# Kernel tuning notes

Hardware: AMD Instinct MI355X
Metric: run time of the kernel (lower is better)

Reference implementation:

```python
import jax, jax.numpy as jnp
import numpy as np

B = 8192
CNN_DIM = 2048
MLP_DIM = 2048
HID = 1024
H = 16
D = HID // H  # 64
EPS = 1e-5


def setup_inputs() -> dict:
    key = jax.random.key(0)
    ks = jax.random.split(key, 12)
    s = 0.02
    return {
        'cnn_out': jax.random.normal(ks[0], (B, CNN_DIM), jnp.float32),
        'mlp_out': jax.random.normal(ks[1], (B, MLP_DIM), jnp.float32),
        # weights stored [in, out] (transposed vs torch nn.Linear)
        'W_cqkv': jax.random.normal(ks[2], (CNN_DIM, 3 * HID), jnp.float32) * s,
        'b_cqkv': jnp.zeros((3 * HID,), jnp.float32),
        'W_mqkv': jax.random.normal(ks[3], (MLP_DIM, 3 * HID), jnp.float32) * s,
        'b_mqkv': jnp.zeros((3 * HID,), jnp.float32),
        'g1': jnp.ones((HID,), jnp.float32),
        'be1': jnp.zeros((HID,), jnp.float32),
        'g2': jnp.ones((HID,), jnp.float32),
        'be2': jnp.zeros((HID,), jnp.float32),
        'W_cproj': jax.random.normal(ks[4], (HID, CNN_DIM), jnp.float32) * s,
        'b_cproj': jnp.zeros((CNN_DIM,), jnp.float32),
        'W_mproj': jax.random.normal(ks[5], (HID, MLP_DIM), jnp.float32) * s,
        'b_mproj': jnp.zeros((MLP_DIM,), jnp.float32),
    }


def _layernorm(x, g, b):
    m = jnp.mean(x, axis=-1, keepdims=True)
    v = jnp.mean((x - m) ** 2, axis=-1, keepdims=True)
    return (x - m) / jnp.sqrt(v + EPS) * g + b


def reference(cnn_out, mlp_out, W_cqkv, b_cqkv, W_mqkv, b_mqkv,
              g1, be1, g2, be2, W_cproj, b_cproj, W_mproj, b_mproj):
    bsz = cnn_out.shape[0]
    scale = 1.0 / jnp.sqrt(jnp.float32(D))

    cqkv = (cnn_out @ W_cqkv + b_cqkv).reshape(bsz, 3, H, D)
    cq, ck, cv = cqkv[:, 0], cqkv[:, 1], cqkv[:, 2]  # each [B,H,D]
    mqkv = (mlp_out @ W_mqkv + b_mqkv).reshape(bsz, 3, H, D)
    mq, mk, mv = mqkv[:, 0], mqkv[:, 1], mqkv[:, 2]

    # branch 1: cnn queries attend over mlp heads -> [B,H,H]
    a1 = jax.nn.softmax(jnp.einsum('bhd,bgd->bhg', cq, mk) * scale, axis=-1)
    ca = jnp.einsum('bhg,bgd->bhd', a1, mv)
    # torch: transpose(1,2).view(B, hidden) -> [B, D, H] flattened
    ca = jnp.swapaxes(ca, 1, 2).reshape(bsz, HID)
    cnn_enh = cnn_out + _layernorm(ca, g1, be1) @ W_cproj + b_cproj

    # branch 2: mlp queries attend over cnn heads
    a2 = jax.nn.softmax(jnp.einsum('bhd,bgd->bhg', mq, ck) * scale, axis=-1)
    ma = jnp.einsum('bhg,bgd->bhd', a2, cv)
    ma = jnp.swapaxes(ma, 1, 2).reshape(bsz, HID)
    mlp_enh = mlp_out + _layernorm(ma, g2, be2) @ W_mproj + b_mproj

    return (cnn_enh, mlp_enh)
```

## Files before the change

kernel.cpp:

```cpp
#include <hip/hip_runtime.h>
#include <hip/hip_bf16.h>
#include <cstdint>
#include <cstddef>

#define NROWS 8192
#define DIM   2048
#define HIDN  1024
#define QKV3  3072
#define EPSV  1e-5f

typedef __attribute__((ext_vector_type(8))) short bf16x8;
typedef __attribute__((ext_vector_type(4))) float f32x4;

__device__ __forceinline__ unsigned short f2bf(float x) {
    __hip_bfloat16 h = __float2bfloat16(x);
    return *reinterpret_cast<unsigned short*>(&h);
}
__device__ __forceinline__ float bf2f(unsigned short u) {
    return __uint_as_float((unsigned)u << 16);
}

__device__ __forceinline__ void gload_lds16(const void* g, void* l) {
    __builtin_amdgcn_global_load_lds(
        (const __attribute__((address_space(1))) void*)g,
        (__attribute__((address_space(3))) void*)l, 16, 0, 0);
}

template <int N> __device__ __forceinline__ void vmwait() {
    if constexpr (N == 8)      asm volatile("s_waitcnt vmcnt(8)" ::: "memory");
    else if constexpr (N == 4) asm volatile("s_waitcnt vmcnt(4)" ::: "memory");
    else if constexpr (N == 2) asm volatile("s_waitcnt vmcnt(2)" ::: "memory");
    else if constexpr (N == 0) asm volatile("s_waitcnt vmcnt(0)" ::: "memory");
}
__device__ __forceinline__ void barrier_mem() {
    asm volatile("s_barrier" ::: "memory");
}

__global__ __launch_bounds__(256) void cvt2_f32_bf16(const float* __restrict__ inA,
                                                     unsigned short* __restrict__ outA,
                                                     const float* __restrict__ inB,
                                                     unsigned short* __restrict__ outB,
                                                     long n) {
    const int which = blockIdx.x >> 13;
    const long bid = blockIdx.x & 8191;
    const float* in = which ? inB : inA;
    unsigned short* out = which ? outB : outA;
    long base = (bid * 256 + threadIdx.x) * 8;
    if (base >= n) return;
    float4 a = *(const float4*)(in + base);
    float4 b = *(const float4*)(in + base + 4);
    uint4 r;
    r.x = (unsigned)f2bf(a.x) | ((unsigned)f2bf(a.y) << 16);
    r.y = (unsigned)f2bf(a.z) | ((unsigned)f2bf(a.w) << 16);
    r.z = (unsigned)f2bf(b.x) | ((unsigned)f2bf(b.y) << 16);
    r.w = (unsigned)f2bf(b.z) | ((unsigned)f2bf(b.w) << 16);
    *(uint4*)(out + base) = r;
}

__global__ __launch_bounds__(256) void cvt_transpose(const float* __restrict__ in,
                                                     unsigned short* __restrict__ out,
                                                     int R, int C) {
    __shared__ float tile[32][33];
    const int tx = threadIdx.x, ty = threadIdx.y;
    const int c0 = blockIdx.x * 32, r0 = blockIdx.y * 32;
#pragma unroll
    for (int i = 0; i < 4; ++i)
        tile[ty + i * 8][tx] = in[(size_t)(r0 + ty + i * 8) * C + c0 + tx];
    __syncthreads();
#pragma unroll
    for (int i = 0; i < 4; ++i)
        out[(size_t)(c0 + ty + i * 8) * R + r0 + tx] = f2bf(tile[tx][ty + i * 8]);
}


__device__ __forceinline__ void stage_half(const unsigned short* __restrict__ G,
                                           int ldK, int rowBase, int kt,
                                           short* ldsHalf, int tid) {
#pragma unroll
    for (int i = 0; i < 2; ++i) {
        const int c = i * 512 + tid;
        const int r = c >> 3;
        const int jl = (c & 7) ^ (r & 7);
        const unsigned short* src = G + (size_t)(rowBase + r) * ldK + kt + jl * 8;
        char* dst = (char*)ldsHalf + (size_t)((i * 512 + (tid & 0x1C0)) * 16);
        gload_lds16(src, dst);
    }
}

__device__ __forceinline__ void load_a4(const short* sAb, int rowA, int o0, int mbase,
                                        bf16x8 (&a)[4][2]) {
#pragma unroll
    for (int m = 0; m < 4; ++m) {
        const char* p = (const char*)sAb + rowA + (mbase + m) * 4096;
        a[m][0] = *(const bf16x8*)(p + o0);
        a[m][1] = *(const bf16x8*)(p + (o0 ^ 64));
    }
}
__device__ __forceinline__ void load_b2(const short* sBb, int rowB, int o0, int nbase,
                                        bf16x8 (&b)[4][2]) {
#pragma unroll
    for (int n = 0; n < 2; ++n) {
        const char* p = (const char*)sBb + rowB + (nbase + n) * 8192;
        b[nbase + n][0] = *(const bf16x8*)(p + o0);
        b[nbase + n][1] = *(const bf16x8*)(p + (o0 ^ 64));
    }
}

#define QUAD(mq, nq)                                                          \
    __builtin_amdgcn_s_setprio(1);                                            \
    _Pragma("unroll") for (int kk_ = 0; kk_ < 2; ++kk_)                       \
    _Pragma("unroll") for (int n_ = 0; n_ < 2; ++n_)                          \
    _Pragma("unroll") for (int m_ = 0; m_ < 4; ++m_)                          \
        acc[(mq) + m_][(nq) + n_] = __builtin_amdgcn_mfma_f32_16x16x32_bf16(  \
            a[m_][kk_], b[(nq) + n_][kk_], acc[(mq) + m_][(nq) + n_], 0, 0, 0); \
    __builtin_amdgcn_s_setprio(0);

#define KTILE(BUF, MODE, KT1, KT2)                                            \
                                                                     \
    load_a4(&sA[BUF][0], rowA, o0, 0, a);                                     \
    if constexpr ((MODE) <= 1)                                                \
        stage_half(Bt, K, tn + 128, (KT1), &sB[(BUF) ^ 1][8192], tid);        \
    if constexpr ((MODE) == 2) { vmwait<2>(); } else { vmwait<8>(); }         \
    barrier_mem();                                                            \
    QUAD(0, 0);                                                               \
                                                                     \
    load_b2(&sB[BUF][0], rowB, o0, 2, b);                                     \
    if constexpr ((MODE) <= 1)                                                \
        stage_half(A, K, tm + 128, (KT1), &sA[(BUF) ^ 1][8192], tid);         \
    if constexpr ((MODE) == 2) { vmwait<0>(); } else { vmwait<8>(); }         \
    barrier_mem();                                                            \
    QUAD(0, 2);                                                               \
                                                                     \
    load_a4(&sA[BUF][0], rowA, o0, 4, a);                                     \
    if constexpr ((MODE) == 0)                                                \
        stage_half(A, K, tm, (KT2), &sA[BUF][0], tid);                        \
    barrier_mem();                                                            \
    QUAD(4, 0);                                                               \
                                                                     \
    if constexpr ((MODE) == 0) {                                              \
        stage_half(Bt, K, tn, (KT2), &sB[BUF][0], tid);                       \
        vmwait<8>();                                                          \
    }                                                                         \
    if constexpr ((MODE) == 1) { vmwait<4>(); }                               \
    barrier_mem();                                                            \
    if constexpr ((MODE) <= 1)                                                \
        load_b2(&sB[(BUF) ^ 1][0], rowB, o0, 0, b);   \
    QUAD(4, 2);

template <int EPI>
__global__ __launch_bounds__(512, 2) void gemm256(
    const unsigned short* __restrict__ A0, const unsigned short* __restrict__ B0t,
    const float* __restrict__ bias0, const float* __restrict__ res0, void* __restrict__ C0,
    const unsigned short* __restrict__ A1, const unsigned short* __restrict__ B1t,
    const float* __restrict__ bias1, const float* __restrict__ res1, void* __restrict__ C1,
    int M, int N, int K, int nbx) {
    __shared__ __align__(16) short sA[2][16384];
    __shared__ __align__(16) short sB[2][16384];

    const int tid = threadIdx.x;
    const int nwg = gridDim.x;
    const int ob = blockIdx.x;
    const int swz = (ob & 7) * (nwg >> 3) + (ob >> 3);
    const int per = nbx * (M >> 8);
    const int which = swz >= per ? 1 : 0;
    const int rem = swz - which * per;
    const int by = rem / nbx, bx = rem % nbx;
    const int tm = by << 8, tn = bx << 8;

    const unsigned short* __restrict__ A  = which ? A1 : A0;
    const unsigned short* __restrict__ Bt = which ? B1t : B0t;
    const float* __restrict__ bias  = which ? bias1 : bias0;
    const float* __restrict__ resid = which ? res1 : res0;

    const int w = tid >> 6, l = tid & 63;
    const int wm = w >> 2, wn = w & 3;
    const int lg = l >> 4, lr = l & 15;
    const int o0 = (lg ^ (lr & 7)) << 4;
    const int rowA = (16 * wm + lr) << 7;
    const int rowB = (16 * wn + lr) << 7;

    f32x4 acc[8][4] = {};
    bf16x8 a[4][2], b[4][2];

    const int T = K >> 6;

    stage_half(A,  K, tm,       0,  &sA[0][0],    tid);
    stage_half(Bt, K, tn,       0,  &sB[0][0],    tid);
    stage_half(Bt, K, tn + 128, 0,  &sB[0][8192], tid);
    stage_half(A,  K, tm + 128, 0,  &sA[0][8192], tid);
    stage_half(A,  K, tm,       64, &sA[1][0],    tid);
    stage_half(Bt, K, tn,       64, &sB[1][0],    tid);
    vmwait<8>();
    barrier_mem();
    load_b2(&sB[0][0], rowB, o0, 0, b);

    int kt = 0;
    for (int tt = 0; tt + 4 <= T; tt += 2) {
        KTILE(0, 0, kt + 64, kt + 128);
        KTILE(1, 0, kt + 128, kt + 192);
        kt += 128;
    }
    KTILE(0, 1, kt + 64, 0);
    KTILE(1, 2, 0, 0);

    const int crow0 = tm + 16 * wm + 4 * lg;
    const int ccol0 = tn + 16 * wn + lr;
    if constexpr (EPI == 0) {
        unsigned short* C = (unsigned short*)(which ? C1 : C0);
#pragma unroll
        for (int mi = 0; mi < 8; ++mi) {
            const int r0 = crow0 + 32 * mi;
#pragma unroll
            for (int ni = 0; ni < 4; ++ni) {
                const int col = ccol0 + 64 * ni;
                const float bb = bias[col];
#pragma unroll
                for (int j = 0; j < 4; ++j)
                    C[(size_t)(r0 + j) * N + col] = f2bf(acc[mi][ni][j] + bb);
            }
        }
    } else {
        float* C = (float*)(which ? C1 : C0);
#pragma unroll
        for (int mi = 0; mi < 8; ++mi) {
            const int r0 = crow0 + 32 * mi;
#pragma unroll
            for (int ni = 0; ni < 4; ++ni) {
                const int col = ccol0 + 64 * ni;
                const float bb = bias[col];
#pragma unroll
                for (int j = 0; j < 4; ++j) {
                    const size_t idx = (size_t)(r0 + j) * N + col;
                    C[idx] = acc[mi][ni][j] + bb + resid[idx];
                }
            }
        }
    }
}

__device__ __forceinline__ void attn_path(const float* __restrict__ q,
                                          const float* __restrict__ k,
                                          const float* __restrict__ v,
                                          const float* __restrict__ gw,
                                          const float* __restrict__ bw,
                                          unsigned short* __restrict__ out, long b,
                                          float* sS, float* sP, float* red, int t) {
    const int h = t >> 4, gg = t & 15;
    const float* qr = q + h * 65;
    const float* kr = k + gg * 65;
    float s = 0.f;
#pragma unroll
    for (int d = 0; d < 64; ++d) s += qr[d] * kr[d];
    sS[t] = s * 0.125f;
    __syncthreads();
    float mx = -1e30f;
#pragma unroll
    for (int j = 0; j < 16; ++j) mx = fmaxf(mx, sS[h * 16 + j]);
    float sum = 0.f;
#pragma unroll
    for (int j = 0; j < 16; ++j) sum += __expf(sS[h * 16 + j] - mx);
    const float aa = __expf(sS[t] - mx) / sum;
    sP[t] = aa;
    __syncthreads();
    float xs[4];
    float lsum = 0.f, lss = 0.f;
#pragma unroll
    for (int r = 0; r < 4; ++r) {
        const int i = t + 256 * r;
        const int d = i >> 4, hh = i & 15;
        float accv = 0.f;
#pragma unroll
        for (int g2 = 0; g2 < 16; ++g2) accv += sP[hh * 16 + g2] * v[g2 * 65 + d];
        xs[r] = accv;
        lsum += accv;
        lss += accv * accv;
    }
#pragma unroll
    for (int off = 32; off > 0; off >>= 1) {
        lsum += __shfl_down(lsum, off);
        lss += __shfl_down(lss, off);
    }
    if ((t & 63) == 0) {
        red[(t >> 6) * 2] = lsum;
        red[(t >> 6) * 2 + 1] = lss;
    }
    __syncthreads();
    const float tot = red[0] + red[2] + red[4] + red[6];
    const float tot2 = red[1] + red[3] + red[5] + red[7];
    const float mean = tot * (1.f / 1024.f);
    const float var = tot2 * (1.f / 1024.f) - mean * mean;
    const float rstd = rsqrtf(var + EPSV);
#pragma unroll
    for (int r = 0; r < 4; ++r) {
        const int i = t + 256 * r;
        const float y = (xs[r] - mean) * rstd * gw[i] + bw[i];
        out[b * 1024 + i] = f2bf(y);
    }
}

__global__ __launch_bounds__(256) void attn_ln(const unsigned short* __restrict__ qkv_c,
                                               const unsigned short* __restrict__ qkv_m,
                                               const float* __restrict__ g1,
                                               const float* __restrict__ be1,
                                               const float* __restrict__ g2,
                                               const float* __restrict__ be2,
                                               unsigned short* __restrict__ ln1,
                                               unsigned short* __restrict__ ln2) {
    __shared__ float qc[48 * 65];
    __shared__ float qm[48 * 65];
    __shared__ float sS[256];
    __shared__ float sP[256];
    __shared__ float red[8];
    const int t = threadIdx.x;
    const long b = blockIdx.x;

    const unsigned short* rc = qkv_c + b * QKV3;
    const unsigned short* rm = qkv_m + b * QKV3;
#pragma unroll
    for (int it = 0; it < 3; ++it) {
        const int i0 = t * 4 + it * 1024;
        ushort4 vc = *(const ushort4*)(rc + i0);
        ushort4 vm = *(const ushort4*)(rm + i0);
        const int o = i0 + (i0 >> 6);
        qc[o + 0] = bf2f(vc.x); qc[o + 1] = bf2f(vc.y);
        qc[o + 2] = bf2f(vc.z); qc[o + 3] = bf2f(vc.w);
        qm[o + 0] = bf2f(vm.x); qm[o + 1] = bf2f(vm.y);
        qm[o + 2] = bf2f(vm.z); qm[o + 3] = bf2f(vm.w);
    }
    __syncthreads();
    attn_path(qc, qm + 16 * 65, qm + 32 * 65, g1, be1, ln1, b, sS, sP, red, t);
    __syncthreads();
    attn_path(qm, qc + 16 * 65, qc + 32 * 65, g2, be2, ln2, b, sS, sP, red, t);
}

extern "C" void kernel_launch(void* const* d_in, const int* in_sizes, int n_in,
                              void* d_out, int out_size, void* d_ws, size_t ws_size,
                              hipStream_t stream) {
    const float* cnn    = (const float*)d_in[0];
    const float* mlp    = (const float*)d_in[1];
    const float* W_cqkv = (const float*)d_in[2];
    const float* b_cqkv = (const float*)d_in[3];
    const float* W_mqkv = (const float*)d_in[4];
    const float* b_mqkv = (const float*)d_in[5];
    const float* g1     = (const float*)d_in[6];
    const float* be1    = (const float*)d_in[7];
    const float* g2     = (const float*)d_in[8];
    const float* be2    = (const float*)d_in[9];
    const float* W_cproj = (const float*)d_in[10];
    const float* b_cproj = (const float*)d_in[11];
    const float* W_mproj = (const float*)d_in[12];
    const float* b_mproj = (const float*)d_in[13];
    float* out = (float*)d_out;
    char* ws = (char*)d_ws;

    unsigned short* Abf_c = (unsigned short*)(ws + 0);
    unsigned short* Abf_m = (unsigned short*)(ws + 33554432);
    unsigned short* WqT_c = (unsigned short*)(ws + 67108864);
    unsigned short* WqT_m = (unsigned short*)(ws + 79691776);
    unsigned short* qkv_c = (unsigned short*)(ws + 92274688);
    unsigned short* qkv_m = (unsigned short*)(ws + 142606336);
    unsigned short* ln1   = (unsigned short*)(ws + 0);
    unsigned short* ln2   = (unsigned short*)(ws + 16777216);
    unsigned short* WpT_c = (unsigned short*)(ws + 33554432);
    unsigned short* WpT_m = (unsigned short*)(ws + 37748736);

    dim3 tb(32, 8);

    cvt2_f32_bf16<<<16384, 256, 0, stream>>>(cnn, Abf_c, mlp, Abf_m, (long)NROWS * DIM);
    cvt_transpose<<<dim3(QKV3 / 32, DIM / 32), tb, 0, stream>>>(W_cqkv, WqT_c, DIM, QKV3);
    cvt_transpose<<<dim3(QKV3 / 32, DIM / 32), tb, 0, stream>>>(W_mqkv, WqT_m, DIM, QKV3);

    gemm256<0><<<768, 512, 0, stream>>>(Abf_c, WqT_c, b_cqkv, nullptr, qkv_c,
                                        Abf_m, WqT_m, b_mqkv, nullptr, qkv_m,
                                        NROWS, QKV3, DIM, QKV3 / 256);

    attn_ln<<<NROWS, 256, 0, stream>>>(qkv_c, qkv_m, g1, be1, g2, be2, ln1, ln2);

    cvt_transpose<<<dim3(DIM / 32, HIDN / 32), tb, 0, stream>>>(W_cproj, WpT_c, HIDN, DIM);
    cvt_transpose<<<dim3(DIM / 32, HIDN / 32), tb, 0, stream>>>(W_mproj, WpT_m, HIDN, DIM);

    gemm256<1><<<512, 512, 0, stream>>>(ln1, WpT_c, b_cproj, cnn, out,
                                        ln2, WpT_m, b_mproj, mlp, out + (size_t)NROWS * DIM,
                                        NROWS, DIM, HIDN, DIM / 256);
}
```

Measured before the change: 416.5 us.

## Use 4-wave 256x256 GEMM tiles with larger per-wave tiles and fuse prep kernels

The GEMM goes from 512 threads (8 waves, 2 blocks per CU) to 256 threads (4 waves, 1 block per CU). Each wave now computes a 128x128 sub-tile with an 8x8 accumulator array, and the A and B fragment loads are reordered across the K-tile pipeline. This raises register reuse and cuts LDS fragment reads per MFMA, at the cost of much higher register pressure and fewer waves to hide latency. Separately, the input conversion and four weight transpose kernels are merged into one prep launch to save launch overhead, and the proj weights move to a separate workspace region.

New measurement: 468.3 us. 12.4% more time.

```diff
diff --git a/kernel.cpp b/kernel.cpp
--- a/kernel.cpp
+++ b/kernel.cpp
@@ -27,42 +27,57 @@
 }
 
 template <int N> __device__ __forceinline__ void vmwait() {
-    if constexpr (N == 8)      asm volatile("s_waitcnt vmcnt(8)" ::: "memory");
+    if constexpr (N == 16)     asm volatile("s_waitcnt vmcnt(16)" ::: "memory");
+    else if constexpr (N == 8) asm volatile("s_waitcnt vmcnt(8)" ::: "memory");
     else if constexpr (N == 4) asm volatile("s_waitcnt vmcnt(4)" ::: "memory");
-    else if constexpr (N == 2) asm volatile("s_waitcnt vmcnt(2)" ::: "memory");
     else if constexpr (N == 0) asm volatile("s_waitcnt vmcnt(0)" ::: "memory");
 }
 __device__ __forceinline__ void barrier_mem() {
     asm volatile("s_barrier" ::: "memory");
 }
 
-__global__ __launch_bounds__(256) void cvt2_f32_bf16(const float* __restrict__ inA,
-                                                     unsigned short* __restrict__ outA,
-                                                     const float* __restrict__ inB,
-                                                     unsigned short* __restrict__ outB,
-                                                     long n) {
-    const int which = blockIdx.x >> 13;
-    const long bid = blockIdx.x & 8191;
-    const float* in = which ? inB : inA;
-    unsigned short* out = which ? outB : outA;
-    long base = (bid * 256 + threadIdx.x) * 8;
-    if (base >= n) return;
-    float4 a = *(const float4*)(in + base);
-    float4 b = *(const float4*)(in + base + 4);
-    uint4 r;
-    r.x = (unsigned)f2bf(a.x) | ((unsigned)f2bf(a.y) << 16);
-    r.y = (unsigned)f2bf(a.z) | ((unsigned)f2bf(a.w) << 16);
-    r.z = (unsigned)f2bf(b.x) | ((unsigned)f2bf(b.y) << 16);
-    r.w = (unsigned)f2bf(b.z) | ((unsigned)f2bf(b.w) << 16);
-    *(uint4*)(out + base) = r;
-}
-
-__global__ __launch_bounds__(256) void cvt_transpose(const float* __restrict__ in,
-                                                     unsigned short* __restrict__ out,
-                                                     int R, int C) {
+__global__ __launch_bounds__(256) void prep(
+    const float* __restrict__ cnn, unsigned short* __restrict__ Abf_c,
+    const float* __restrict__ mlp, unsigned short* __restrict__ Abf_m,
+    const float* __restrict__ Wcq, unsigned short* __restrict__ WqT_c,
+    const float* __restrict__ Wmq, unsigned short* __restrict__ WqT_m,
+    const float* __restrict__ Wcp, unsigned short* __restrict__ WpT_c,
+    const float* __restrict__ Wmp, unsigned short* __restrict__ WpT_m) {
     __shared__ float tile[32][33];
-    const int tx = threadIdx.x, ty = threadIdx.y;
-    const int c0 = blockIdx.x * 32, r0 = blockIdx.y * 32;
+    const int bid = blockIdx.x;
+    const int t = threadIdx.x;
+    if (bid < 16384) {
+        const int which = bid >> 13;
+        const long b = bid & 8191;
+        const float* in = which ? mlp : cnn;
+        unsigned short* out = which ? Abf_m : Abf_c;
+        const long base = (b * 256 + t) * 8;
+        float4 a = *(const float4*)(in + base);
+        float4 v = *(const float4*)(in + base + 4);
+        uint4 r;
+        r.x = (unsigned)f2bf(a.x) | ((unsigned)f2bf(a.y) << 16);
+        r.y = (unsigned)f2bf(a.z) | ((unsigned)f2bf(a.w) << 16);
+        r.z = (unsigned)f2bf(v.x) | ((unsigned)f2bf(v.y) << 16);
+        r.w = (unsigned)f2bf(v.z) | ((unsigned)f2bf(v.w) << 16);
+        *(uint4*)(out + base) = r;
+        return;
+    }
+    const int tx = t & 31, ty = t >> 5;
+    const float* in;
+    unsigned short* out;
+    int R, C, l, gw;
+    if (bid < 28672) {
+        l = bid - 16384;
+        const int wq = l / 6144;
+        l -= wq * 6144;
+        in = wq ? Wmq : Wcq; out = wq ? WqT_m : WqT_c; R = DIM; C = QKV3; gw = 96;
+    } else {
+        l = bid - 28672;
+        const int wp = l / 2048;
+        l -= wp * 2048;
+        in = wp ? Wmp : Wcp; out = wp ? WpT_m : WpT_c; R = HIDN; C = DIM; gw = 64;
+    }
+    const int c0 = (l % gw) * 32, r0 = (l / gw) * 32;
 #pragma unroll
     for (int i = 0; i < 4; ++i)
         tile[ty + i * 8][tx] = in[(size_t)(r0 + ty + i * 8) * C + c0 + tx];
@@ -77,78 +92,70 @@
                                            int ldK, int rowBase, int kt,
                                            short* ldsHalf, int tid) {
 #pragma unroll
-    for (int i = 0; i < 2; ++i) {
-        const int c = i * 512 + tid;
+    for (int i = 0; i < 4; ++i) {
+        const int c = i * 256 + tid;
         const int r = c >> 3;
         const int jl = (c & 7) ^ (r & 7);
         const unsigned short* src = G + (size_t)(rowBase + r) * ldK + kt + jl * 8;
-        char* dst = (char*)ldsHalf + (size_t)((i * 512 + (tid & 0x1C0)) * 16);
+        char* dst = (char*)ldsHalf + (size_t)((i * 256 + (tid & 0xC0)) * 16);
         gload_lds16(src, dst);
     }
 }
 
-__device__ __forceinline__ void load_a4(const short* sAb, int rowA, int o0, int mbase,
-                                        bf16x8 (&a)[4][2]) {
+__device__ __forceinline__ void load_f4(const short* base, int rowOff, int o0,
+                                        int tbase, bf16x8 (&d)[4][2]) {
 #pragma unroll
     for (int m = 0; m < 4; ++m) {
-        const char* p = (const char*)sAb + rowA + (mbase + m) * 4096;
-        a[m][0] = *(const bf16x8*)(p + o0);
-        a[m][1] = *(const bf16x8*)(p + (o0 ^ 64));
-    }
-}
-__device__ __forceinline__ void load_b2(const short* sBb, int rowB, int o0, int nbase,
-                                        bf16x8 (&b)[4][2]) {
-#pragma unroll
-    for (int n = 0; n < 2; ++n) {
-        const char* p = (const char*)sBb + rowB + (nbase + n) * 8192;
-        b[nbase + n][0] = *(const bf16x8*)(p + o0);
-        b[nbase + n][1] = *(const bf16x8*)(p + (o0 ^ 64));
-    }
-}
-
-#define QUAD(mq, nq)                                                          \
+        const char* p = (const char*)base + rowOff + (tbase + m) * 4096;
+        d[m][0] = *(const bf16x8*)(p + o0);
+        d[m][1] = *(const bf16x8*)(p + (o0 ^ 64));
+    }
+}
+
+#define QUAD(mq, nq, BSET)                                                    \
     __builtin_amdgcn_s_setprio(1);                                            \
     _Pragma("unroll") for (int kk_ = 0; kk_ < 2; ++kk_)                       \
-    _Pragma("unroll") for (int n_ = 0; n_ < 2; ++n_)                          \
+    _Pragma("unroll") for (int n_ = 0; n_ < 4; ++n_)                          \
     _Pragma("unroll") for (int m_ = 0; m_ < 4; ++m_)                          \
         acc[(mq) + m_][(nq) + n_] = __builtin_amdgcn_mfma_f32_16x16x32_bf16(  \
-            a[m_][kk_], b[(nq) + n_][kk_], acc[(mq) + m_][(nq) + n_], 0, 0, 0); \
+            a[m_][kk_], BSET[n_][kk_], acc[(mq) + m_][(nq) + n_], 0, 0, 0);   \
     __builtin_amdgcn_s_setprio(0);
 
 #define KTILE(BUF, MODE, KT1, KT2)                                            \
                                                                      \
-    load_a4(&sA[BUF][0], rowA, o0, 0, a);                                     \
     if constexpr ((MODE) <= 1)                                                \
         stage_half(Bt, K, tn + 128, (KT1), &sB[(BUF) ^ 1][8192], tid);        \
-    if constexpr ((MODE) == 2) { vmwait<2>(); } else { vmwait<8>(); }         \
+    if constexpr ((MODE) == 2) { vmwait<4>(); } else { vmwait<16>(); }        \
     barrier_mem();                                                            \
-    QUAD(0, 0);                                                               \
+    QUAD(0, 0, bL);                                                           \
                                                                      \
-    load_b2(&sB[BUF][0], rowB, o0, 2, b);                                     \
+    load_f4(&sB[BUF][0], rowB, o0, 4, bH);                                    \
     if constexpr ((MODE) <= 1)                                                \
         stage_half(A, K, tm + 128, (KT1), &sA[(BUF) ^ 1][8192], tid);         \
-    if constexpr ((MODE) == 2) { vmwait<0>(); } else { vmwait<8>(); }         \
+    if constexpr ((MODE) == 2) { vmwait<0>(); } else { vmwait<16>(); }        \
     barrier_mem();                                                            \
-    QUAD(0, 2);                                                               \
+    QUAD(0, 4, bH);                                                           \
                                                                      \
-    load_a4(&sA[BUF][0], rowA, o0, 4, a);                                     \
+    load_f4(&sA[BUF][0], rowA, o0, 4, a);                                     \
     if constexpr ((MODE) == 0)                                                \
         stage_half(A, K, tm, (KT2), &sA[BUF][0], tid);                        \
     barrier_mem();                                                            \
-    QUAD(4, 0);                                                               \
+    QUAD(4, 4, bH);                                                           \
                                                                      \
     if constexpr ((MODE) == 0) {                                              \
         stage_half(Bt, K, tn, (KT2), &sB[BUF][0], tid);                       \
-        vmwait<8>();                                                          \
+        vmwait<16>();                                                         \
     }                                                                         \
-    if constexpr ((MODE) == 1) { vmwait<4>(); }                               \
+    if constexpr ((MODE) == 1) { vmwait<8>(); }                               \
     barrier_mem();                                                            \
-    if constexpr ((MODE) <= 1)                                                \
-        load_b2(&sB[(BUF) ^ 1][0], rowB, o0, 0, b);   \
-    QUAD(4, 2);
+    QUAD(4, 0, bL);                                                           \
+    if constexpr ((MODE) <= 1) {                                              \
+        load_f4(&sA[(BUF) ^ 1][0], rowA, o0, 0, a);             \
+        load_f4(&sB[(BUF) ^ 1][0], rowB, o0, 0, bL);            \
+    }
 
 template <int EPI>
-__global__ __launch_bounds__(512, 2) void gemm256(
+__global__ __launch_bounds__(256, 1) void gemm256(
     const unsigned short* __restrict__ A0, const unsigned short* __restrict__ B0t,
     const float* __restrict__ bias0, const float* __restrict__ res0, void* __restrict__ C0,
     const unsigned short* __restrict__ A1, const unsigned short* __restrict__ B1t,
@@ -173,14 +180,14 @@
     const float* __restrict__ resid = which ? res1 : res0;
 
     const int w = tid >> 6, l = tid & 63;
-    const int wm = w >> 2, wn = w & 3;
+    const int wm = w >> 1, wn = w & 1;
     const int lg = l >> 4, lr = l & 15;
     const int o0 = (lg ^ (lr & 7)) << 4;
     const int rowA = (16 * wm + lr) << 7;
     const int rowB = (16 * wn + lr) << 7;
 
-    f32x4 acc[8][4] = {};
-    bf16x8 a[4][2], b[4][2];
+    f32x4 acc[8][8] = {};
+    bf16x8 a[4][2], bL[4][2], bH[4][2];
 
     const int T = K >> 6;
 
@@ -190,9 +197,10 @@
     stage_half(A,  K, tm + 128, 0,  &sA[0][8192], tid);
     stage_half(A,  K, tm,       64, &sA[1][0],    tid);
     stage_half(Bt, K, tn,       64, &sB[1][0],    tid);
-    vmwait<8>();
+    vmwait<16>();
     barrier_mem();
-    load_b2(&sB[0][0], rowB, o0, 0, b);
+    load_f4(&sA[0][0], rowA, o0, 0, a);
+    load_f4(&sB[0][0], rowB, o0, 0, bL);
 
     int kt = 0;
     for (int tt = 0; tt + 4 <= T; tt += 2) {
@@ -211,8 +219,8 @@
         for (int mi = 0; mi < 8; ++mi) {
             const int r0 = crow0 + 32 * mi;
 #pragma unroll
-            for (int ni = 0; ni < 4; ++ni) {
-                const int col = ccol0 + 64 * ni;
+            for (int ni = 0; ni < 8; ++ni) {
+                const int col = ccol0 + 32 * ni;
                 const float bb = bias[col];
 #pragma unroll
                 for (int j = 0; j < 4; ++j)
@@ -225,8 +233,8 @@
         for (int mi = 0; mi < 8; ++mi) {
             const int r0 = crow0 + 32 * mi;
 #pragma unroll
-            for (int ni = 0; ni < 4; ++ni) {
-                const int col = ccol0 + 64 * ni;
+            for (int ni = 0; ni < 8; ++ni) {
+                const int col = ccol0 + 32 * ni;
                 const float bb = bias[col];
 #pragma unroll
                 for (int j = 0; j < 4; ++j) {
@@ -361,25 +369,20 @@
     unsigned short* qkv_m = (unsigned short*)(ws + 142606336);
     unsigned short* ln1   = (unsigned short*)(ws + 0);
     unsigned short* ln2   = (unsigned short*)(ws + 16777216);
-    unsigned short* WpT_c = (unsigned short*)(ws + 33554432);
-    unsigned short* WpT_m = (unsigned short*)(ws + 37748736);
-
-    dim3 tb(32, 8);
-
-    cvt2_f32_bf16<<<16384, 256, 0, stream>>>(cnn, Abf_c, mlp, Abf_m, (long)NROWS * DIM);
-    cvt_transpose<<<dim3(QKV3 / 32, DIM / 32), tb, 0, stream>>>(W_cqkv, WqT_c, DIM, QKV3);
-    cvt_transpose<<<dim3(QKV3 / 32, DIM / 32), tb, 0, stream>>>(W_mqkv, WqT_m, DIM, QKV3);
-
-    gemm256<0><<<768, 512, 0, stream>>>(Abf_c, WqT_c, b_cqkv, nullptr, qkv_c,
+    unsigned short* WpT_c = (unsigned short*)(ws + 192937984);
+    unsigned short* WpT_m = (unsigned short*)(ws + 197132288);
+
+    prep<<<32768, 256, 0, stream>>>(cnn, Abf_c, mlp, Abf_m,
+                                    W_cqkv, WqT_c, W_mqkv, WqT_m,
+                                    W_cproj, WpT_c, W_mproj, WpT_m);
+
+    gemm256<0><<<768, 256, 0, stream>>>(Abf_c, WqT_c, b_cqkv, nullptr, qkv_c,
                                         Abf_m, WqT_m, b_mqkv, nullptr, qkv_m,
                                         NROWS, QKV3, DIM, QKV3 / 256);
 
     attn_ln<<<NROWS, 256, 0, stream>>>(qkv_c, qkv_m, g1, be1, g2, be2, ln1, ln2);
 
-    cvt_transpose<<<dim3(DIM / 32, HIDN / 32), tb, 0, stream>>>(W_cproj, WpT_c, HIDN, DIM);
-    cvt_transpose<<<dim3(DIM / 32, HIDN / 32), tb, 0, stream>>>(W_mproj, WpT_m, HIDN, DIM);
-
-    gemm256<1><<<512, 512, 0, stream>>>(ln1, WpT_c, b_cproj, cnn, out,
+    gemm256<1><<<512, 256, 0, stream>>>(ln1, WpT_c, b_cproj, cnn, out,
                                         ln2, WpT_m, b_mproj, mlp, out + (size_t)NROWS * DIM,
                                         NROWS, DIM, HIDN, DIM / 256);
 }
```
